# Optimization experiments

Hardware: AMD Instinct MI355X
Metric: run time of the kernel (lower is better)

## Reference

```python
import jax, jax.numpy as jnp
import numpy as np

N_LAYERS = 2   # number of S6 blocks
D = 512        # input_dim / d_model
N = 16         # hid_dim (SSM state size)
O = 512        # output_dim
B = 4          # batch
L = 2048       # seq_len
LN_EPS = 1e-5


def setup_inputs() -> dict:
    key = jax.random.key(0)
    ks = jax.random.split(key, 10)
    s = D ** -0.5
    inp = {
        "x": jax.random.normal(ks[0], (B, L, D), jnp.float32),
        # per-layer S6 block params (stacked over layer axis)
        "A_log": jax.random.normal(ks[1], (N_LAYERS, D, N), jnp.float32) * 0.5,
        "W_B": jax.random.normal(ks[2], (N_LAYERS, D, N), jnp.float32) * s,
        "b_B": jnp.zeros((N_LAYERS, N), jnp.float32),
        "W_C": jax.random.normal(ks[3], (N_LAYERS, D, N), jnp.float32) * s,
        "b_C": jnp.zeros((N_LAYERS, N), jnp.float32),
        "W_dt": jax.random.normal(ks[4], (N_LAYERS, D, D), jnp.float32) * s,
        "b_dt": jnp.zeros((N_LAYERS, D), jnp.float32),
        "D_skip": jnp.ones((N_LAYERS, D), jnp.float32),
        # mixing linear + layer norm per layer
        "W_mix": jax.random.normal(ks[5], (N_LAYERS, D, D), jnp.float32) * s,
        "b_mix": jnp.zeros((N_LAYERS, D), jnp.float32),
        "ln_g": jnp.ones((N_LAYERS, D), jnp.float32),
        "ln_b": jnp.zeros((N_LAYERS, D), jnp.float32),
        # final decoder
        "W_dec": jax.random.normal(ks[6], (D, O), jnp.float32) * s,
        "b_dec": jnp.zeros((O,), jnp.float32),
    }
    return inp


def _combine(e1, e2):
    # first-order linear recurrence combine: h <- a*h + u
    a1, u1 = e1
    a2, u2 = e2
    return a1 * a2, a2 * u1 + u2


def reference(x, A_log, W_B, b_B, W_C, b_C, W_dt, b_dt, D_skip,
              W_mix, b_mix, ln_g, ln_b, W_dec, b_dec):
    h_in = x  # [B, L, D]
    for i in range(N_LAYERS):
        # ---- S6 block: input-dependent B, C, dt; diagonal A ----
        A = -jnp.exp(A_log[i])                               # [D, N], negative real
        Bm = h_in @ W_B[i] + b_B[i]                          # [B, L, N]
        Cm = h_in @ W_C[i] + b_C[i]                          # [B, L, N]
        dt = jax.nn.softplus(h_in @ W_dt[i] + b_dt[i])       # [B, L, D]
        # discretize: a_t = exp(dt*A), u_t = dt * B_t * x_t
        a = jnp.exp(dt[..., None] * A)                       # [B, L, D, N]
        u = (dt * h_in)[..., None] * Bm[:, :, None, :]       # [B, L, D, N]
        # parallel scan over sequence axis (Heinsen / Blelloch style)
        _, h = jax.lax.associative_scan(_combine, (a, u), axis=1)
        y = jnp.einsum('bln,bldn->bld', Cm, h) + D_skip[i] * h_in  # [B, L, D]
        # ---- activation (torch.nn.GELU default = exact erf) ----
        y = jax.nn.gelu(y, approximate=False)
        # ---- mixing linear ----
        y = y @ W_mix[i] + b_mix[i]
        # ---- layer norm ----
        mu = jnp.mean(y, axis=-1, keepdims=True)
        var = jnp.var(y, axis=-1, keepdims=True)
        y = (y - mu) / jnp.sqrt(var + LN_EPS) * ln_g[i] + ln_b[i]
        # ---- residual ----
        h_in = h_in + y
    return h_in @ W_dec + b_dec  # [B, L, O]
```

## Files before the change

### kernel.cpp

```cpp
#include <hip/hip_runtime.h>
#include <math.h>

typedef unsigned short u16;
typedef unsigned int u32;
typedef __attribute__((ext_vector_type(8))) _Float16 half8;
typedef __attribute__((ext_vector_type(4))) float f32x4;

#define BL 8192
#define DD 512
#define NN 16
#define NCHUNK 64
#define SCH 32
#define ZLD 640

__device__ __forceinline__ float softplus_f(float z) {
  float w = __builtin_amdgcn_exp2f(-1.4426950408889634f * fabsf(z));
  return fmaxf(z, 0.0f) + 0.69314718055994531f * __builtin_amdgcn_logf(1.0f + w);
}

__device__ __forceinline__ float gelu_erf(float y) {
  float ax = fabsf(y) * 0.70710678118654752f;
  float t  = __builtin_amdgcn_rcpf(1.0f + 0.3275911f * ax);
  float e  = __builtin_amdgcn_exp2f(-1.4426950408889634f * ax * ax);
  float p  = ((((1.061405429f * t - 1.453152027f) * t + 1.421413741f) * t
               - 0.284496736f) * t + 0.254829592f) * t;
  float er = copysignf(1.0f - p * e, y);
  return 0.5f * y * (1.0f + er);
}

#define PREP_TOT (4194304 + 655360 + 524288 + 262144 + 1280 + 16384)
__global__ __launch_bounds__(256) void prep_kernel(
    const float* __restrict__ x, const float* __restrict__ A_log,
    const float* __restrict__ W_B, const float* __restrict__ b_B,
    const float* __restrict__ W_C, const float* __restrict__ b_C,
    const float* __restrict__ W_dt, const float* __restrict__ b_dt,
    const float* __restrict__ W_mix, const float* __restrict__ W_dec,
    _Float16* __restrict__ x16, _Float16* __restrict__ Wc16,
    _Float16* __restrict__ Wm16, _Float16* __restrict__ Wd16,
    float* __restrict__ bcat, float* __restrict__ A2)
{
  int i = blockIdx.x * 256 + threadIdx.x;
  if (i >= PREP_TOT) return;
  if (i < 4194304) { x16[i] = (_Float16)x[i]; return; }
  i -= 4194304;
  if (i < 655360) {
    int l = i / 327680, r = i % 327680, n = r >> 9, k = r & 511;
    float v = 0.0f;
    if (n < 16)       v = W_B[l * 8192 + k * 16 + n];
    else if (n < 32)  v = W_C[l * 8192 + k * 16 + (n - 16)];
    else if (n < 544) v = W_dt[l * 262144 + k * 512 + (n - 32)];
    Wc16[i] = (_Float16)v;
    return;
  }
  i -= 655360;
  if (i < 524288) {
    int l = i / 262144, r = i % 262144, n = r >> 9, k = r & 511;
    Wm16[i] = (_Float16)W_mix[l * 262144 + k * 512 + n];
    return;
  }
  i -= 524288;
  if (i < 262144) {
    int n = i >> 9, k = i & 511;
    Wd16[i] = (_Float16)W_dec[k * 512 + n];
    return;
  }
  i -= 262144;
  if (i < 1280) {
    int l = i / 640, n = i % 640;
    float v = 0.0f;
    if (n < 16)       v = b_B[l * 16 + n];
    else if (n < 32)  v = b_C[l * 16 + (n - 16)];
    else if (n < 544) v = b_dt[l * 512 + (n - 32)];
    bcat[i] = v;
    return;
  }
  i -= 1280;
  A2[i] = -expf(A_log[i]) * 1.4426950408889634f;
}

template <int MODE>
__global__ __launch_bounds__(256) void gemm_f16(
    const _Float16* __restrict__ A, const _Float16* __restrict__ Bt,
    const float* __restrict__ bias, float* __restrict__ Cmat, int ldc)
{
  const int K = 512;
  int bid = blockIdx.x;
  int xcd = bid & 7;
  int rest = bid >> 3;
  int mloc = rest & 7;
  int nb = rest >> 3;
  int m0 = (xcd * 8 + mloc) * 128;
  int n0 = nb * 64;
  __shared__ __align__(16) char smem[36864];
  _Float16* As = (_Float16*)smem;
  _Float16* Bs = As + 128 * 64;
  int tid = threadIdx.x;
  int wave = tid >> 6, lane = tid & 63;
  int wm = (wave >> 1) * 64;
  int wn = (wave & 1) * 32;
  int lrow = lane & 15;
  int q4 = lane >> 4;
  f32x4 acc[4][2] = {};

  int srow = tid >> 3;
  int scol = ((tid & 7) ^ (srow & 7)) * 8;
  size_t gA = (size_t)(m0 + srow) * K + scol;
  size_t gB = (size_t)(n0 + srow) * K + scol;
  unsigned sdst = (unsigned)(wave * 512);

  for (int k0 = 0; k0 < K; k0 += 64) {
#pragma unroll
    for (int j = 0; j < 4; ++j)
      __builtin_amdgcn_global_load_lds(
          (const __attribute__((address_space(1))) void*)(A + gA + (size_t)(j * 32) * K + k0),
          (__attribute__((address_space(3))) void*)(&As[j * 2048 + sdst]), 16, 0, 0);
#pragma unroll
    for (int j = 0; j < 2; ++j)
      __builtin_amdgcn_global_load_lds(
          (const __attribute__((address_space(1))) void*)(Bt + gB + (size_t)(j * 32) * K + k0),
          (__attribute__((address_space(3))) void*)(&Bs[j * 2048 + sdst]), 16, 0, 0);
    __syncthreads();
#pragma unroll
    for (int kk = 0; kk < 2; ++kk) {
      half8 af[4], bf[2];
#pragma unroll
      for (int i = 0; i < 4; ++i) {
        int r = wm + i * 16 + lrow;
        int cb = (kk * 4 + q4) ^ (lrow & 7);
        af[i] = *(const half8*)&As[r * 64 + cb * 8];
      }
#pragma unroll
      for (int t = 0; t < 2; ++t) {
        int r = wn + t * 16 + lrow;
        int cb = (kk * 4 + q4) ^ (lrow & 7);
        bf[t] = *(const half8*)&Bs[r * 64 + cb * 8];
      }
#pragma unroll
      for (int i = 0; i < 4; ++i)
#pragma unroll
        for (int t = 0; t < 2; ++t)
          acc[i][t] = __builtin_amdgcn_mfma_f32_16x16x32_f16(af[i], bf[t], acc[i][t], 0, 0, 0);
    }
    __syncthreads();
  }

  float* ct = (float*)smem + wave * (64 * 36);
#pragma unroll
  for (int t = 0; t < 2; ++t) {
    int coll = wn + t * 16 + lrow;
    float bv = bias[n0 + coll];
    bool sp = (MODE == 1) && (n0 + coll >= 32);
#pragma unroll
    for (int i = 0; i < 4; ++i) {
#pragma unroll
      for (int r = 0; r < 4; ++r) {
        float v = acc[i][t][r] + bv;
        if (sp) v = softplus_f(v);
        ct[(i * 16 + q4 * 4 + r) * 36 + (t * 16 + lrow)] = v;
      }
    }
  }
  __syncthreads();
  int r8 = lane >> 3, c8 = lane & 7;
  int colv = n0 + wn + c8 * 4;
  bool do_store = !(MODE == 1 && colv >= 544);
#pragma unroll
  for (int pass = 0; pass < 8; ++pass) {
    int rowl = pass * 8 + r8;
    float4 v = *(const float4*)&ct[rowl * 36 + c8 * 4];
    if (do_store)
      *(float4*)&Cmat[(size_t)(m0 + wm + rowl) * ldc + colv] = v;
  }
}

template <int PACKED>
__global__ __launch_bounds__(256) void scan_p1(
    const float* __restrict__ Z, const float* __restrict__ Xf,
    const _Float16* __restrict__ Xh, const float* __restrict__ A2,
    float* __restrict__ Ach, float* __restrict__ Uch)
{
  int bid = blockIdx.x;
  int dg = bid & 1, c = (bid >> 1) & (NCHUNK - 1), b = bid >> 7;
  int d = dg * 256 + threadIdx.x;
  int row0 = b * 2048 + c * SCH;
  __shared__ float Bsh[SCH * 16];
  for (int i = threadIdx.x; i < SCH * 16; i += 256)
    Bsh[i] = Z[(size_t)(row0 + (i >> 4)) * ZLD + (i & 15)];
  __syncthreads();
  float a2[16];
  const float4* a2v = (const float4*)(A2 + d * 16);
#pragma unroll
  for (int q = 0; q < 4; ++q) {
    float4 f = a2v[q];
    a2[q * 4 + 0] = f.x; a2[q * 4 + 1] = f.y; a2[q * 4 + 2] = f.z; a2[q * 4 + 3] = f.w;
  }
  float ap[16], u[16];
#pragma unroll
  for (int n = 0; n < 16; ++n) { ap[n] = 1.0f; u[n] = 0.0f; }
  for (int t = 0; t < SCH; ++t) {
    size_t row = row0 + t;
    float dtv = Z[row * ZLD + 32 + d];
    float xv = PACKED ? (float)Xh[row * DD + d] : Xf[row * DD + d];
    float dx = dtv * xv;
#pragma unroll
    for (int n = 0; n < 16; ++n) {
      float e = __builtin_amdgcn_exp2f(dtv * a2[n]);
      u[n] = e * u[n] + dx * Bsh[t * 16 + n];
      ap[n] *= e;
    }
  }
  size_t out = ((size_t)(b * NCHUNK + c) * DD + d) * 16;
#pragma unroll
  for (int n = 0; n < 16; ++n) { Ach[out + n] = ap[n]; Uch[out + n] = u[n]; }
}

__global__ __launch_bounds__(256) void scan_p2(
    const float* __restrict__ Ach, float* __restrict__ Uch)
{
  int blk = blockIdx.x;
  int b = blk >> 7;
  int dn = (blk & 127) * 64 + (threadIdx.x & 63);
  int seg = threadIdx.x >> 6;
  size_t base = (size_t)b * NCHUNK * 8192 + dn;
  float a_r[16], u_r[16];
#pragma unroll
  for (int i = 0; i < 16; ++i) {
    size_t idx = base + (size_t)(seg * 16 + i) * 8192;
    a_r[i] = Ach[idx];
    u_r[i] = Uch[idx];
  }
  float Ap = 1.0f, hA = 0.0f;
#pragma unroll
  for (int i = 0; i < 16; ++i) { hA = a_r[i] * hA + u_r[i]; Ap *= a_r[i]; }
  __shared__ float AsegL[4][64], UsegL[4][64];
  AsegL[seg][threadIdx.x & 63] = Ap;
  UsegL[seg][threadIdx.x & 63] = hA;
  __syncthreads();
  float h = 0.0f;
  for (int s = 0; s < seg; ++s)
    h = AsegL[s][threadIdx.x & 63] * h + UsegL[s][threadIdx.x & 63];
#pragma unroll
  for (int i = 0; i < 16; ++i) {
    size_t idx = base + (size_t)(seg * 16 + i) * 8192;
    Uch[idx] = h;
    h = a_r[i] * h + u_r[i];
  }
}

template <int PACKED>
__global__ __launch_bounds__(256) void scan_p3(
    const float* __restrict__ Z, const float* __restrict__ Xf,
    const _Float16* __restrict__ Xh, const float* __restrict__ A2,
    const float* __restrict__ Hinit, const float* __restrict__ Dskip,
    _Float16* __restrict__ Yout)
{
  int bid = blockIdx.x;
  int dg = bid & 1, c = (bid >> 1) & (NCHUNK - 1), b = bid >> 7;
  int d = dg * 256 + threadIdx.x;
  int row0 = b * 2048 + c * SCH;
  __shared__ float Bsh[SCH * 16];
  __shared__ float Csh[SCH * 16];
  for (int i = threadIdx.x; i < SCH * 16; i += 256) {
    size_t rz = (size_t)(row0 + (i >> 4)) * ZLD;
    Bsh[i] = Z[rz + (i & 15)];
    Csh[i] = Z[rz + 16 + (i & 15)];
  }
  __syncthreads();
  float a2[16];
  const float4* a2v = (const float4*)(A2 + d * 16);
#pragma unroll
  for (int q = 0; q < 4; ++q) {
    float4 f = a2v[q];
    a2[q * 4 + 0] = f.x; a2[q * 4 + 1] = f.y; a2[q * 4 + 2] = f.z; a2[q * 4 + 3] = f.w;
  }
  float h[16];
  size_t hidx = ((size_t)(b * NCHUNK + c) * DD + d) * 16;
#pragma unroll
  for (int n = 0; n < 16; ++n) h[n] = Hinit[hidx + n];
  float dsk = Dskip[d];
  for (int t = 0; t < SCH; ++t) {
    size_t row = row0 + t;
    float dtv = Z[row * ZLD + 32 + d];
    float xv = PACKED ? (float)Xh[row * DD + d] : Xf[row * DD + d];
    float dx = dtv * xv;
    float acc = 0.0f;
#pragma unroll
    for (int n = 0; n < 16; ++n) {
      float e = __builtin_amdgcn_exp2f(dtv * a2[n]);
      h[n] = e * h[n] + dx * Bsh[t * 16 + n];
      acc += Csh[t * 16 + n] * h[n];
    }
    float y = acc + dsk * xv;
    Yout[row * DD + d] = (_Float16)gelu_erf(y);
  }
}

template <int PACKED>
__global__ __launch_bounds__(256) void ln_residual(
    const float* __restrict__ Y2, const float* Xf,
    const float* __restrict__ gam, const float* __restrict__ bet,
    _Float16* Hh)
{
  int wave = threadIdx.x >> 6, lane = threadIdx.x & 63;
  size_t row = (size_t)blockIdx.x * 4 + wave;
  size_t gbase = row * DD + lane * 8;
  const float4* yr = (const float4*)(Y2 + gbase);
  float4 y0 = yr[0], y1 = yr[1];
  float v[8] = {y0.x, y0.y, y0.z, y0.w, y1.x, y1.y, y1.z, y1.w};
  float s = 0.0f, sq = 0.0f;
#pragma unroll
  for (int j = 0; j < 8; ++j) { s += v[j]; sq += v[j] * v[j]; }
#pragma unroll
  for (int off = 32; off; off >>= 1) {
    s += __shfl_xor(s, off, 64);
    sq += __shfl_xor(sq, off, 64);
  }
  float mu = s * (1.0f / 512.0f);
  float var = sq * (1.0f / 512.0f) - mu * mu;
  float rstd = rsqrtf(var + 1e-5f);

  float hin[8];
  if (PACKED) {
    half8 hh = *(const half8*)(Hh + gbase);
#pragma unroll
    for (int j = 0; j < 8; ++j) hin[j] = (float)hh[j];
  } else {
    const float4* xr = (const float4*)(Xf + gbase);
    float4 x0 = xr[0], x1 = xr[1];
    hin[0]=x0.x; hin[1]=x0.y; hin[2]=x0.z; hin[3]=x0.w;
    hin[4]=x1.x; hin[5]=x1.y; hin[6]=x1.z; hin[7]=x1.w;
  }
  const float4* g4 = (const float4*)(gam + lane * 8);
  const float4* b4 = (const float4*)(bet + lane * 8);
  float4 g0 = g4[0], g1 = g4[1], bb0 = b4[0], bb1 = b4[1];
  float gv[8] = {g0.x,g0.y,g0.z,g0.w,g1.x,g1.y,g1.z,g1.w};
  float bv[8] = {bb0.x,bb0.y,bb0.z,bb0.w,bb1.x,bb1.y,bb1.z,bb1.w};
  half8 sh;
#pragma unroll
  for (int j = 0; j < 8; ++j) {
    float o = (v[j] - mu) * rstd * gv[j] + bv[j] + hin[j];
    sh[j] = (_Float16)o;
  }
  *(half8*)(Hh + gbase) = sh;
}

extern "C" void kernel_launch(void* const* d_in, const int* in_sizes, int n_in,
                              void* d_out, int out_size, void* d_ws, size_t ws_size,
                              hipStream_t stream) {
  const float* x      = (const float*)d_in[0];
  const float* A_log  = (const float*)d_in[1];
  const float* W_B    = (const float*)d_in[2];
  const float* b_B    = (const float*)d_in[3];
  const float* W_C    = (const float*)d_in[4];
  const float* b_C    = (const float*)d_in[5];
  const float* W_dt   = (const float*)d_in[6];
  const float* b_dt   = (const float*)d_in[7];
  const float* D_skip = (const float*)d_in[8];
  const float* W_mix  = (const float*)d_in[9];
  const float* b_mix  = (const float*)d_in[10];
  const float* ln_g   = (const float*)d_in[11];
  const float* ln_b   = (const float*)d_in[12];
  const float* W_dec  = (const float*)d_in[13];
  const float* b_dec  = (const float*)d_in[14];

  char* ws = (char*)d_ws;
  size_t off = 0;
  _Float16* x16 = (_Float16*)(ws + off);
  float*    Ach = (float*)(ws + off);     off += 8388608;
  _Float16* y16 = (_Float16*)(ws + off);  off += 8388608;
  _Float16* h16 = (_Float16*)(ws + off);  off += 8388608;
  float* Z    = (float*)(ws + off);
  float* y2   = (float*)(ws + off); off += 20971520;
  float* Uch  = (float*)(ws + off); off += 8388608;
  _Float16* Wc16 = (_Float16*)(ws + off); off += 1310720;
  _Float16* Wm16 = (_Float16*)(ws + off); off += 1048576;
  _Float16* Wd16 = (_Float16*)(ws + off); off += 524288;
  float* bcat = (float*)(ws + off); off += 5120;
  float* A2w  = (float*)(ws + off); off += 65536;

  prep_kernel<<<(PREP_TOT + 255) / 256, 256, 0, stream>>>(
      x, A_log, W_B, b_B, W_C, b_C, W_dt, b_dt, W_mix, W_dec,
      x16, Wc16, Wm16, Wd16, bcat, A2w);

  for (int l = 0; l < 2; ++l) {
    const _Float16* Ain = (l == 0) ? x16 : h16;
    gemm_f16<1><<<576, 256, 0, stream>>>(
        Ain, Wc16 + l * 640 * 512, bcat + l * 640, Z, ZLD);
    if (l == 0) {
      scan_p1<0><<<512, 256, 0, stream>>>(Z, x, nullptr,
                                          A2w + l * 8192, Ach, Uch);
      scan_p2<<<512, 256, 0, stream>>>(Ach, Uch);
      scan_p3<0><<<512, 256, 0, stream>>>(Z, x, nullptr, A2w + l * 8192,
                                          Uch, D_skip + l * 512, y16);
    } else {
      scan_p1<1><<<512, 256, 0, stream>>>(Z, nullptr, h16,
                                          A2w + l * 8192, Ach, Uch);
      scan_p2<<<512, 256, 0, stream>>>(Ach, Uch);
      scan_p3<1><<<512, 256, 0, stream>>>(Z, nullptr, h16, A2w + l * 8192,
                                          Uch, D_skip + l * 512, y16);
    }
    gemm_f16<0><<<512, 256, 0, stream>>>(
        y16, Wm16 + l * 512 * 512, b_mix + l * 512, y2, DD);
    if (l == 0)
      ln_residual<0><<<2048, 256, 0, stream>>>(y2, x, ln_g + l * 512,
                                               ln_b + l * 512, h16);
    else
      ln_residual<1><<<2048, 256, 0, stream>>>(y2, nullptr, ln_g + l * 512,
                                               ln_b + l * 512, h16);
  }
  gemm_f16<0><<<512, 256, 0, stream>>>(
      h16, Wd16, b_dec, (float*)d_out, DD);
}
```

Before: 281.7 us.

## Fuse mixing GEMM with layernorm and residual; read fp16 input in scans

Adds gemm_mix_ln, where each 512-thread block computes a full 32x512 output row tile, reduces LN statistics in registers and shared memory, then writes normalized output plus residual as fp16. This drops the fp32 y2 intermediate and the separate ln_residual launch. The layer-0 scans now read the fp16 x16 copy instead of fp32 x, and the GEMM swizzle index now uses the full row. Only 256 blocks are launched, so the fused GEMM may have low occupancy and little latency hiding.

```diff
diff --git a/kernel.cpp b/kernel.cpp
--- a/kernel.cpp
+++ b/kernel.cpp
@@ -4,6 +4,7 @@
 typedef unsigned short u16;
 typedef unsigned int u32;
 typedef __attribute__((ext_vector_type(8))) _Float16 half8;
+typedef __attribute__((ext_vector_type(4))) _Float16 half4;
 typedef __attribute__((ext_vector_type(4))) float f32x4;
 
 #define BL 8192
@@ -12,6 +13,9 @@
 #define NCHUNK 64
 #define SCH 32
 #define ZLD 640
+
+#define AS1(p) (const __attribute__((address_space(1))) void*)(p)
+#define AS3(p) (__attribute__((address_space(3))) void*)(p)
 
 __device__ __forceinline__ float softplus_f(float z) {
   float w = __builtin_amdgcn_exp2f(-1.4426950408889634f * fabsf(z));
@@ -112,13 +116,13 @@
 #pragma unroll
     for (int j = 0; j < 4; ++j)
       __builtin_amdgcn_global_load_lds(
-          (const __attribute__((address_space(1))) void*)(A + gA + (size_t)(j * 32) * K + k0),
-          (__attribute__((address_space(3))) void*)(&As[j * 2048 + sdst]), 16, 0, 0);
+          AS1(A + gA + (size_t)(j * 32) * K + k0),
+          AS3(&As[j * 2048 + sdst]), 16, 0, 0);
 #pragma unroll
     for (int j = 0; j < 2; ++j)
       __builtin_amdgcn_global_load_lds(
-          (const __attribute__((address_space(1))) void*)(Bt + gB + (size_t)(j * 32) * K + k0),
-          (__attribute__((address_space(3))) void*)(&Bs[j * 2048 + sdst]), 16, 0, 0);
+          AS1(Bt + gB + (size_t)(j * 32) * K + k0),
+          AS3(&Bs[j * 2048 + sdst]), 16, 0, 0);
     __syncthreads();
 #pragma unroll
     for (int kk = 0; kk < 2; ++kk) {
@@ -126,13 +130,13 @@
 #pragma unroll
       for (int i = 0; i < 4; ++i) {
         int r = wm + i * 16 + lrow;
-        int cb = (kk * 4 + q4) ^ (lrow & 7);
+        int cb = (kk * 4 + q4) ^ (r & 7);
         af[i] = *(const half8*)&As[r * 64 + cb * 8];
       }
 #pragma unroll
       for (int t = 0; t < 2; ++t) {
         int r = wn + t * 16 + lrow;
-        int cb = (kk * 4 + q4) ^ (lrow & 7);
+        int cb = (kk * 4 + q4) ^ (r & 7);
         bf[t] = *(const half8*)&Bs[r * 64 + cb * 8];
       }
 #pragma unroll
@@ -173,10 +177,152 @@
   }
 }
 
-template <int PACKED>
+template <int RES_PACKED>
+__global__ __launch_bounds__(512) void gemm_mix_ln(
+    const _Float16* __restrict__ A, const _Float16* __restrict__ Bt,
+    const float* __restrict__ bias, const float* __restrict__ gam,
+    const float* __restrict__ bet, const float* __restrict__ Xf,
+    _Float16* __restrict__ H)
+{
+  const int K = 512;
+  int m0 = blockIdx.x * 32;
+  __shared__ __align__(16) char smem[34816 + 32 * 8 * 2 * 4 + 32 * 2 * 4];
+  _Float16* As = (_Float16*)smem;
+  _Float16* Bs = As + 32 * 32;
+  float* stats = (float*)(smem + 34816);
+  float* mv    = stats + 32 * 8 * 2;
+  int tid = threadIdx.x;
+  int wave = tid >> 6, lane = tid & 63;
+  int lrow = lane & 15, q4 = lane >> 4;
+  int wn = wave * 64;
+  f32x4 acc[2][4] = {};
+
+  int rA = tid >> 2, sA = tid & 3;
+  size_t gA = (size_t)(m0 + rA) * K + ((sA ^ ((rA >> 1) & 3)) * 8);
+  size_t gB[4]; unsigned dB[4];
+#pragma unroll
+  for (int j = 0; j < 4; ++j) {
+    int c = j * 512 + tid;
+    int r = c >> 2, s = c & 3;
+    gB[j] = (size_t)r * K + ((s ^ ((r >> 1) & 3)) * 8);
+    dB[j] = c * 8;
+  }
+
+  for (int k0 = 0; k0 < K; k0 += 32) {
+    if (wave < 2)
+      __builtin_amdgcn_global_load_lds(AS1(A + gA + k0), AS3(As + tid * 8), 16, 0, 0);
+#pragma unroll
+    for (int j = 0; j < 4; ++j)
+      __builtin_amdgcn_global_load_lds(AS1(Bt + gB[j] + k0), AS3(Bs + dB[j]), 16, 0, 0);
+    __syncthreads();
+    half8 af[2], bf[4];
+#pragma unroll
+    for (int i = 0; i < 2; ++i) {
+      int r = i * 16 + lrow;
+      af[i] = *(const half8*)&As[r * 32 + ((q4 ^ ((r >> 1) & 3)) * 8)];
+    }
+#pragma unroll
+    for (int t = 0; t < 4; ++t) {
+      int n = wn + t * 16 + lrow;
+      bf[t] = *(const half8*)&Bs[n * 32 + ((q4 ^ ((n >> 1) & 3)) * 8)];
+    }
+#pragma unroll
+    for (int i = 0; i < 2; ++i)
+#pragma unroll
+      for (int t = 0; t < 4; ++t)
+        acc[i][t] = __builtin_amdgcn_mfma_f32_16x16x32_f16(af[i], bf[t], acc[i][t], 0, 0, 0);
+    __syncthreads();
+  }
+
+  float bv[4], gv[4], betv[4];
+#pragma unroll
+  for (int t = 0; t < 4; ++t) {
+    int col = wn + t * 16 + lrow;
+    bv[t] = bias[col]; gv[t] = gam[col]; betv[t] = bet[col];
+  }
+
+#pragma unroll
+  for (int i = 0; i < 2; ++i)
+#pragma unroll
+    for (int rr = 0; rr < 4; ++rr) {
+      float s = 0.0f, sq = 0.0f;
+#pragma unroll
+      for (int t = 0; t < 4; ++t) {
+        float v = acc[i][t][rr] + bv[t];
+        s += v; sq += v * v;
+      }
+#pragma unroll
+      for (int off = 8; off; off >>= 1) {
+        s += __shfl_xor(s, off, 64);
+        sq += __shfl_xor(sq, off, 64);
+      }
+      if (lrow == 0) {
+        int row = i * 16 + q4 * 4 + rr;
+        stats[row * 16 + wave * 2 + 0] = s;
+        stats[row * 16 + wave * 2 + 1] = sq;
+      }
+    }
+  __syncthreads();
+  if (tid < 32) {
+    float s = 0.0f, sq = 0.0f;
+#pragma unroll
+    for (int w = 0; w < 8; ++w) {
+      s += stats[tid * 16 + w * 2 + 0];
+      sq += stats[tid * 16 + w * 2 + 1];
+    }
+    float mu = s * (1.0f / 512.0f);
+    float var = sq * (1.0f / 512.0f) - mu * mu;
+    mv[tid * 2 + 0] = mu;
+    mv[tid * 2 + 1] = rsqrtf(var + 1e-5f);
+  }
+  __syncthreads();
+
+  float* patch = (float*)smem;
+#pragma unroll
+  for (int half = 0; half < 2; ++half) {
+    if ((wave >> 2) == half) {
+      float* pw = patch + (wave & 3) * (32 * 68);
+#pragma unroll
+      for (int i = 0; i < 2; ++i)
+#pragma unroll
+        for (int rr = 0; rr < 4; ++rr) {
+          int row = i * 16 + q4 * 4 + rr;
+          float mu = mv[row * 2 + 0], rstd = mv[row * 2 + 1];
+#pragma unroll
+          for (int t = 0; t < 4; ++t) {
+            float v = acc[i][t][rr] + bv[t];
+            pw[row * 68 + t * 16 + lrow] = (v - mu) * rstd * gv[t] + betv[t];
+          }
+        }
+    }
+    __syncthreads();
+#pragma unroll
+    for (int p = 0; p < 4; ++p) {
+      int idx = p * 512 + tid;
+      int row = idx >> 6, c = idx & 63;
+      int w4 = c >> 4, c16 = c & 15;
+      float4 v = *(const float4*)&patch[w4 * (32 * 68) + row * 68 + c16 * 4];
+      size_t g = (size_t)(m0 + row) * DD + (half * 4 + w4) * 64 + c16 * 4;
+      float r0, r1, r2, r3;
+      if (RES_PACKED) {
+        half4 hr = *(const half4*)(H + g);
+        r0 = (float)hr[0]; r1 = (float)hr[1]; r2 = (float)hr[2]; r3 = (float)hr[3];
+      } else {
+        float4 fr = *(const float4*)(Xf + g);
+        r0 = fr.x; r1 = fr.y; r2 = fr.z; r3 = fr.w;
+      }
+      half4 hv;
+      hv[0] = (_Float16)(v.x + r0); hv[1] = (_Float16)(v.y + r1);
+      hv[2] = (_Float16)(v.z + r2); hv[3] = (_Float16)(v.w + r3);
+      *(half4*)(H + g) = hv;
+    }
+    __syncthreads();
+  }
+}
+
 __global__ __launch_bounds__(256) void scan_p1(
-    const float* __restrict__ Z, const float* __restrict__ Xf,
-    const _Float16* __restrict__ Xh, const float* __restrict__ A2,
+    const float* __restrict__ Z, const _Float16* __restrict__ Xh,
+    const float* __restrict__ A2,
     float* __restrict__ Ach, float* __restrict__ Uch)
 {
   int bid = blockIdx.x;
@@ -200,7 +346,7 @@
   for (int t = 0; t < SCH; ++t) {
     size_t row = row0 + t;
     float dtv = Z[row * ZLD + 32 + d];
-    float xv = PACKED ? (float)Xh[row * DD + d] : Xf[row * DD + d];
+    float xv = (float)Xh[row * DD + d];
     float dx = dtv * xv;
 #pragma unroll
     for (int n = 0; n < 16; ++n) {
@@ -247,12 +393,10 @@
   }
 }
 
-template <int PACKED>
 __global__ __launch_bounds__(256) void scan_p3(
-    const float* __restrict__ Z, const float* __restrict__ Xf,
-    const _Float16* __restrict__ Xh, const float* __restrict__ A2,
-    const float* __restrict__ Hinit, const float* __restrict__ Dskip,
-    _Float16* __restrict__ Yout)
+    const float* __restrict__ Z, const _Float16* __restrict__ Xh,
+    const float* __restrict__ A2, const float* __restrict__ Hinit,
+    const float* __restrict__ Dskip, _Float16* __restrict__ Yout)
 {
   int bid = blockIdx.x;
   int dg = bid & 1, c = (bid >> 1) & (NCHUNK - 1), b = bid >> 7;
@@ -281,7 +425,7 @@
   for (int t = 0; t < SCH; ++t) {
     size_t row = row0 + t;
     float dtv = Z[row * ZLD + 32 + d];
-    float xv = PACKED ? (float)Xh[row * DD + d] : Xf[row * DD + d];
+    float xv = (float)Xh[row * DD + d];
     float dx = dtv * xv;
     float acc = 0.0f;
 #pragma unroll
@@ -293,55 +437,6 @@
     float y = acc + dsk * xv;
     Yout[row * DD + d] = (_Float16)gelu_erf(y);
   }
-}
-
-template <int PACKED>
-__global__ __launch_bounds__(256) void ln_residual(
-    const float* __restrict__ Y2, const float* Xf,
-    const float* __restrict__ gam, const float* __restrict__ bet,
-    _Float16* Hh)
-{
-  int wave = threadIdx.x >> 6, lane = threadIdx.x & 63;
-  size_t row = (size_t)blockIdx.x * 4 + wave;
-  size_t gbase = row * DD + lane * 8;
-  const float4* yr = (const float4*)(Y2 + gbase);
-  float4 y0 = yr[0], y1 = yr[1];
-  float v[8] = {y0.x, y0.y, y0.z, y0.w, y1.x, y1.y, y1.z, y1.w};
-  float s = 0.0f, sq = 0.0f;
-#pragma unroll
-  for (int j = 0; j < 8; ++j) { s += v[j]; sq += v[j] * v[j]; }
-#pragma unroll
-  for (int off = 32; off; off >>= 1) {
-    s += __shfl_xor(s, off, 64);
-    sq += __shfl_xor(sq, off, 64);
-  }
-  float mu = s * (1.0f / 512.0f);
-  float var = sq * (1.0f / 512.0f) - mu * mu;
-  float rstd = rsqrtf(var + 1e-5f);
-
-  float hin[8];
-  if (PACKED) {
-    half8 hh = *(const half8*)(Hh + gbase);
-#pragma unroll
-    for (int j = 0; j < 8; ++j) hin[j] = (float)hh[j];
-  } else {
-    const float4* xr = (const float4*)(Xf + gbase);
-    float4 x0 = xr[0], x1 = xr[1];
-    hin[0]=x0.x; hin[1]=x0.y; hin[2]=x0.z; hin[3]=x0.w;
-    hin[4]=x1.x; hin[5]=x1.y; hin[6]=x1.z; hin[7]=x1.w;
-  }
-  const float4* g4 = (const float4*)(gam + lane * 8);
-  const float4* b4 = (const float4*)(bet + lane * 8);
-  float4 g0 = g4[0], g1 = g4[1], bb0 = b4[0], bb1 = b4[1];
-  float gv[8] = {g0.x,g0.y,g0.z,g0.w,g1.x,g1.y,g1.z,g1.w};
-  float bv[8] = {bb0.x,bb0.y,bb0.z,bb0.w,bb1.x,bb1.y,bb1.z,bb1.w};
-  half8 sh;
-#pragma unroll
-  for (int j = 0; j < 8; ++j) {
-    float o = (v[j] - mu) * rstd * gv[j] + bv[j] + hin[j];
-    sh[j] = (_Float16)o;
-  }
-  *(half8*)(Hh + gbase) = sh;
 }
 
 extern "C" void kernel_launch(void* const* d_in, const int* in_sizes, int n_in,
@@ -365,12 +460,11 @@
 
   char* ws = (char*)d_ws;
   size_t off = 0;
-  _Float16* x16 = (_Float16*)(ws + off);
-  float*    Ach = (float*)(ws + off);     off += 8388608;
+  _Float16* x16 = (_Float16*)(ws + off);  off += 8388608;
   _Float16* y16 = (_Float16*)(ws + off);  off += 8388608;
   _Float16* h16 = (_Float16*)(ws + off);  off += 8388608;
-  float* Z    = (float*)(ws + off);
-  float* y2   = (float*)(ws + off); off += 20971520;
+  float* Z    = (float*)(ws + off); off += 20971520;
+  float* Ach  = (float*)(ws + off); off += 8388608;
   float* Uch  = (float*)(ws + off); off += 8388608;
   _Float16* Wc16 = (_Float16*)(ws + off); off += 1310720;
   _Float16* Wm16 = (_Float16*)(ws + off); off += 1048576;
@@ -386,27 +480,17 @@
     const _Float16* Ain = (l == 0) ? x16 : h16;
     gemm_f16<1><<<576, 256, 0, stream>>>(
         Ain, Wc16 + l * 640 * 512, bcat + l * 640, Z, ZLD);
-    if (l == 0) {
-      scan_p1<0><<<512, 256, 0, stream>>>(Z, x, nullptr,
-                                          A2w + l * 8192, Ach, Uch);
-      scan_p2<<<512, 256, 0, stream>>>(Ach, Uch);
-      scan_p3<0><<<512, 256, 0, stream>>>(Z, x, nullptr, A2w + l * 8192,
-                                          Uch, D_skip + l * 512, y16);
-    } else {
-      scan_p1<1><<<512, 256, 0, stream>>>(Z, nullptr, h16,
-                                          A2w + l * 8192, Ach, Uch);
-      scan_p2<<<512, 256, 0, stream>>>(Ach, Uch);
-      scan_p3<1><<<512, 256, 0, stream>>>(Z, nullptr, h16, A2w + l * 8192,
-                                          Uch, D_skip + l * 512, y16);
-    }
-    gemm_f16<0><<<512, 256, 0, stream>>>(
-        y16, Wm16 + l * 512 * 512, b_mix + l * 512, y2, DD);
+    scan_p1<<<512, 256, 0, stream>>>(Z, Ain, A2w + l * 8192, Ach, Uch);
+    scan_p2<<<512, 256, 0, stream>>>(Ach, Uch);
+    scan_p3<<<512, 256, 0, stream>>>(Z, Ain, A2w + l * 8192, Uch,
+                                     D_skip + l * 512, y16);
     if (l == 0)
-      ln_residual<0><<<2048, 256, 0, stream>>>(y2, x, ln_g + l * 512,
-                                               ln_b + l * 512, h16);
+      gemm_mix_ln<0><<<256, 512, 0, stream>>>(
+          y16, Wm16, b_mix, ln_g, ln_b, x, h16);
     else
-      ln_residual<1><<<2048, 256, 0, stream>>>(y2, nullptr, ln_g + l * 512,
-                                               ln_b + l * 512, h16);
+      gemm_mix_ln<1><<<256, 512, 0, stream>>>(
+          y16, Wm16 + 262144, b_mix + 512, ln_g + 512, ln_b + 512,
+          nullptr, h16);
   }
   gemm_f16<0><<<512, 256, 0, stream>>>(
       h16, Wd16, b_dec, (float*)d_out, DD);
```

After: 290.9 us. 3.3% more time.
